# Kernel tuning notes

Measured on AMD Instinct MI355X. Metric: run time of the kernel, lower is better.

## Reference

```python
import jax, jax.numpy as jnp
import numpy as np

NUM_HEADS = 8
NUM_LEVEL = 4
KERNEL = 2
NUM_POINT = KERNEL * KERNEL
D_MODEL = 256
HEAD_DIM = D_MODEL // NUM_HEADS
REF_SIZE = 4
EPS = 1e-6


def _kernel_indices():
    # even kernel: linspace(-k/2+0.5, k/2-0.5, k) -> [-0.5, 0.5] for k=2
    ind = np.linspace(-KERNEL // 2 + 0.5, KERNEL // 2 - 0.5, KERNEL)
    i, j = np.meshgrid(ind, ind, indexing='ij')
    ki = np.stack([j, i], axis=-1).reshape(-1, 2) / KERNEL  # (P, 2), (x, y)
    return jnp.asarray(ki, dtype=jnp.float32)


def _ref_windows(shapes):
    # mask is None -> centers on a regular grid, size = ref_size / (H, W)
    refs = []
    for (H, W) in shapes:
        y = (jnp.arange(1, H + 1, dtype=jnp.float32) - 0.5) / (H + EPS)
        x = (jnp.arange(1, W + 1, dtype=jnp.float32) - 0.5) / (W + EPS)
        yy, xx = jnp.meshgrid(y, x, indexing='ij')           # (H, W)
        center = jnp.stack([xx, yy], axis=-1).reshape(-1, 2)  # (HW, 2)
        size = jnp.broadcast_to(
            jnp.array([REF_SIZE / W, REF_SIZE / H], dtype=jnp.float32), center.shape)
        refs.append(jnp.concatenate([center, size], axis=-1))
    return jnp.concatenate(refs, axis=0)  # (L, 4)


def _bilinear_sample(vflat, grid, H, W):
    """vflat: (B, H*W, M, D) one level; grid: (B, Lq, M, P, 2) normalized [0,1].
    Returns (B, Lq, M, P, D). Zero padding outside, align_corners=False."""
    B, _, M, D = vflat.shape
    x = grid[..., 0] * W - 0.5
    y = grid[..., 1] * H - 0.5
    x0 = jnp.floor(x); y0 = jnp.floor(y)
    lx = x - x0; ly = y - y0
    x0i = x0.astype(jnp.int32); y0i = y0.astype(jnp.int32)
    bidx = jnp.arange(B)[:, None, None, None]
    midx = jnp.arange(M)[None, None, :, None]

    def corner(xi, yi, w):
        valid = (xi >= 0) & (xi < W) & (yi >= 0) & (yi < H)
        idx = jnp.clip(yi, 0, H - 1) * W + jnp.clip(xi, 0, W - 1)
        g = vflat[bidx, idx, midx]  # (B, Lq, M, P, D)
        return g * (w * valid.astype(w.dtype))[..., None]

    out = corner(x0i, y0i, (1 - lx) * (1 - ly))
    out = out + corner(x0i + 1, y0i, lx * (1 - ly))
    out = out + corner(x0i, y0i + 1, (1 - lx) * ly)
    out = out + corner(x0i + 1, y0i + 1, lx * ly)
    return out


def setup_inputs() -> dict:
    key = jax.random.key(0)
    ks = jax.random.split(key, 20)
    spatial = [(100, 100), (50, 50), (25, 25), (13, 13)]
    B = 4
    inp = {}
    for i, (H, W) in enumerate(spatial):
        inp[f'value{i}'] = jax.random.normal(ks[i], (B, D_MODEL, H, W), dtype=jnp.float32)
        inp[f'pos{i}'] = jax.random.normal(ks[4 + i], (B, D_MODEL, H, W), dtype=jnp.float32)
    s = 0.05
    inp['Wv'] = jax.random.normal(ks[8], (D_MODEL, D_MODEL), dtype=jnp.float32) * s
    inp['bv'] = jnp.zeros((D_MODEL,), dtype=jnp.float32)
    inp['Wo'] = jax.random.normal(ks[9], (D_MODEL, D_MODEL), dtype=jnp.float32) * s
    inp['bo'] = jnp.zeros((D_MODEL,), dtype=jnp.float32)
    nb = NUM_LEVEL * NUM_HEADS * 4
    inp['Wbox'] = jax.random.normal(ks[10], (nb, D_MODEL), dtype=jnp.float32) * s
    inp['bbox'] = jax.random.uniform(ks[11], (nb,), dtype=jnp.float32)
    na = NUM_HEADS * NUM_LEVEL * NUM_POINT
    inp['Wattn'] = jax.random.normal(ks[12], (na, D_MODEL), dtype=jnp.float32) * s
    inp['battn'] = jax.random.normal(ks[13], (na,), dtype=jnp.float32) * s
    return inp


def reference(value0, value1, value2, value3, pos0, pos1, pos2, pos3,
              Wv, bv, Wo, bo, Wbox, bbox, Wattn, battn):
    levels = [value0, value1, value2, value3]
    poss = [pos0, pos1, pos2, pos3]
    shapes = [(v.shape[2], v.shape[3]) for v in levels]
    B = levels[0].shape[0]

    # flatten pyramid: (B, C, H, W) -> (B, HW, C)
    value = jnp.concatenate(
        [v.reshape(B, D_MODEL, -1).transpose(0, 2, 1) for v in levels], axis=1)
    pos = jnp.concatenate(
        [p.reshape(B, D_MODEL, -1).transpose(0, 2, 1) for p in poss], axis=1)
    L = value.shape[1]

    query = value + pos
    vp = (value @ Wv.T + bv).reshape(B, L, NUM_HEADS, HEAD_DIM)

    attn = jax.nn.softmax(
        (query @ Wattn.T + battn).reshape(B, L, NUM_HEADS, NUM_LEVEL * NUM_POINT),
        axis=-1).reshape(B, L, NUM_HEADS, NUM_LEVEL, NUM_POINT)

    offset = (query @ Wbox.T + bbox).reshape(B, L, NUM_HEADS, NUM_LEVEL, 4)
    ref = _ref_windows(shapes)[None, :, None, None, :]          # (1, L, 1, 1, 4)
    boxes = ref + offset / 8.0 * ref[..., jnp.array([2, 3, 2, 3])]
    center = boxes[..., None, :2]                               # (B, L, M, NL, 1, 2)
    size = boxes[..., None, 2:]
    ki = _kernel_indices()[None, None, None, None, :, :]        # (1,1,1,1,P,2)
    grid = center + ki * jax.nn.relu(size)                      # (B, L, M, NL, P, 2)

    out = jnp.zeros((B, L, NUM_HEADS, HEAD_DIM), dtype=vp.dtype)
    start = 0
    for l, (H, W) in enumerate(shapes):
        end = start + H * W
        vf = vp[:, start:end]                                   # (B, HW, M, D)
        sampled = _bilinear_sample(vf, grid[:, :, :, l], H, W)  # (B, L, M, P, D)
        out = out + jnp.einsum('blmp,blmpd->blmd', attn[:, :, :, l], sampled)
        start = end

    return out.reshape(B, L, D_MODEL) @ Wo.T + bo
```

## Files before the change

### kernel.cpp

```cpp
#include <hip/hip_runtime.h>
#include <cstdint>
#include <cmath>

#define D_MODEL 256
#define NH 8
#define NLVL 4
#define LTOT 13294
#define BATCH 4
#define BTOT (BATCH * LTOT)
#define RPAD 53248

typedef __attribute__((ext_vector_type(8))) short bf8;
typedef __attribute__((ext_vector_type(4))) float f4;
typedef __attribute__((ext_vector_type(2))) float f2;

__device__ __forceinline__ unsigned short f2bf(float x) {
    unsigned u = __float_as_uint(x);
    u += 0x7fffu + ((u >> 16) & 1u);
    return (unsigned short)(u >> 16);
}
__device__ __forceinline__ float bf2f(unsigned short h) {
    return __uint_as_float(((unsigned)h) << 16);
}
__device__ __forceinline__ f2 up2(unsigned u) {
    return (f2){__uint_as_float(u << 16), __uint_as_float(u & 0xffff0000u)};
}
__device__ __forceinline__ int swzf(int i, int s) { return s ^ ((i >> 1) & 3); }
__device__ __forceinline__ int xcd_swz(int hw, int nwg) {
    int xcd = hw & 7, k = hw >> 3;
    int q = nwg >> 3, r = nwg & 7;
    return (xcd < r ? xcd * (q + 1) : r * (q + 1) + (xcd - r) * q) + k;
}

__device__ __forceinline__ void level_of(int l, int& lv, int& hw, int& Wl, int& HWl, int& loff) {
    if (l < 10000)      { lv = 0; loff = 0;     Wl = 100; HWl = 10000; }
    else if (l < 12500) { lv = 1; loff = 10000; Wl = 50;  HWl = 2500;  }
    else if (l < 13125) { lv = 2; loff = 12500; Wl = 25;  HWl = 625;   }
    else                { lv = 3; loff = 13125; Wl = 13;  HWl = 169;   }
    hw = l - loff;
}

__global__ __launch_bounds__(256) void pack_weights(
    const float* __restrict__ Wv, const float* __restrict__ Wattn,
    const float* __restrict__ Wbox, const float* __restrict__ Wo,
    unsigned short* __restrict__ W1hi, unsigned short* __restrict__ W1lo,
    unsigned short* __restrict__ Wohi, unsigned short* __restrict__ Wolo) {
    int tid = blockIdx.x * 256 + threadIdx.x;
    const float* src;
    unsigned short *dh, *dl;
    int nb, kb, j, s;
    if (tid < 16384) {
        nb = tid >> 12; kb = (tid >> 9) & 7; j = (tid >> 2) & 127; s = tid & 3;
        int f = nb * 128 + j, c0 = kb * 32 + s * 8;
        if (f < 256)      src = Wv + (size_t)f * 256 + c0;
        else if (f < 384) src = Wattn + (size_t)(f - 256) * 256 + c0;
        else              src = Wbox + (size_t)(f - 384) * 256 + c0;
        dh = W1hi; dl = W1lo;
    } else if (tid < 24576) {
        int t2 = tid - 16384;
        nb = t2 >> 12; kb = (t2 >> 9) & 7; j = (t2 >> 2) & 127; s = t2 & 3;
        int f = nb * 128 + j, c0 = kb * 32 + s * 8;
        src = Wo + (size_t)f * 256 + c0;
        dh = Wohi; dl = Wolo;
    } else return;
    int base = (((nb * 8 + kb) * 128 + j) * 4 + swzf(j, s)) * 8;
    #pragma unroll
    for (int e = 0; e < 8; ++e) {
        float x = src[e];
        unsigned short h = f2bf(x);
        dh[base + e] = h;
        dl[base + e] = f2bf(x - bf2f(h));
    }
}

__global__ __launch_bounds__(256) void convert_A(
    const float* __restrict__ v0, const float* __restrict__ v1,
    const float* __restrict__ v2, const float* __restrict__ v3,
    const float* __restrict__ p0, const float* __restrict__ p1,
    const float* __restrict__ p2, const float* __restrict__ p3,
    unsigned short* __restrict__ Gv, unsigned short* __restrict__ Gq) {
    __shared__ unsigned short HV[64][130];
    __shared__ unsigned short HQ[64][130];
    int t = threadIdx.x;
    int w = t >> 6, lane = t & 63;
    int r0 = blockIdx.x * 64;

    int r = r0 + lane; if (r >= BTOT) r = BTOT - 1;
    int b = r / LTOT, l = r % LTOT;
    int lv, hw, Wl, HWl, loff;
    level_of(l, lv, hw, Wl, HWl, loff);
    const float *vb, *pb;
    switch (lv) { case 0: vb = v0; pb = p0; break; case 1: vb = v1; pb = p1; break;
                  case 2: vb = v2; pb = p2; break; default: vb = v3; pb = p3; break; }
    size_t base = (size_t)b * D_MODEL * (size_t)HWl + (size_t)hw;
    vb += base; pb += base;

    int kb2 = (lane >> 2) & 3, slot = lane & 3;
    for (int h = 0; h < 2; ++h) {
        #pragma unroll 4
        for (int i = 0; i < 32; ++i) {
            int cl = i * 4 + w;
            int c = h * 128 + cl;
            float av = vb[(size_t)c * HWl];
            float aq = av + pb[(size_t)c * HWl];
            HV[lane][cl] = f2bf(av);
            HQ[lane][cl] = f2bf(aq);
        }
        __syncthreads();
        #pragma unroll
        for (int j = 0; j < 8; ++j) {
            int plane = j >> 2;
            int rl = (j & 3) * 16 + w * 4 + (lane >> 4);
            int oct = slot ^ ((rl >> 1) & 3);
            const unsigned* s32 = (const unsigned*)(plane ? &HQ[rl][kb2 * 32 + oct * 8]
                                                          : &HV[rl][kb2 * 32 + oct * 8]);
            uint4 vst = make_uint4(s32[0], s32[1], s32[2], s32[3]);
            unsigned short* dst = (plane ? Gq : Gv)
                + (size_t)(r0 + rl) * 256 + (h * 4 + kb2) * 32 + slot * 8;
            *(uint4*)dst = vst;
        }
        __syncthreads();
    }
}

__global__ __launch_bounds__(512, 4) void gemm1_mfma(
    const unsigned short* __restrict__ Gv, const unsigned short* __restrict__ Gq,
    const unsigned short* __restrict__ W1hi, const unsigned short* __restrict__ W1lo,
    const float* __restrict__ bv, const float* __restrict__ battn, const float* __restrict__ bbox,
    unsigned short* __restrict__ VPb, float* __restrict__ LB) {
    __shared__ __align__(16) unsigned short Ah[2][8192], Bh[2][4096], Bl[2][4096];
    int t = threadIdx.x;
    int lid = xcd_swz(blockIdx.x, 4 * (RPAD / 256));
    int nb = lid & 3;
    int r0 = (lid >> 2) * 256;
    const unsigned short* Asrc = (nb < 2) ? Gv : Gq;
    int w = t >> 6, lane = t & 63;
    int wr = w >> 1, wc = w & 1;
    int row_l = lane & 15, oct = lane >> 4;

    const unsigned short* Bbh = W1hi + (size_t)nb * 32768;
    const unsigned short* Bbl = W1lo + (size_t)nb * 32768;

    f4 acc[4][4];
    #pragma unroll
    for (int i = 0; i < 4; ++i)
        #pragma unroll
        for (int j = 0; j < 4; ++j) acc[i][j] = (f4){0.f, 0.f, 0.f, 0.f};

    int c0 = t, c1 = t + 512;
    const unsigned short* a0b = Asrc + (size_t)(r0 + (c0 >> 2)) * 256 + (c0 & 3) * 8;
    const unsigned short* a1b = Asrc + (size_t)(r0 + (c1 >> 2)) * 256 + (c1 & 3) * 8;

#define G1_STAGE(bb, kb)                                                            \
    {                                                                               \
        __builtin_amdgcn_global_load_lds(a0b + (kb) * 32, &Ah[bb][w * 512], 16, 0, 0);        \
        __builtin_amdgcn_global_load_lds(a1b + (kb) * 32, &Ah[bb][4096 + w * 512], 16, 0, 0); \
        __builtin_amdgcn_global_load_lds(Bbh + (kb) * 4096 + c0 * 8, &Bh[bb][w * 512], 16, 0, 0); \
        __builtin_amdgcn_global_load_lds(Bbl + (kb) * 4096 + c0 * 8, &Bl[bb][w * 512], 16, 0, 0); \
    }

    G1_STAGE(0, 0);
    for (int kb = 0; kb < 8; ++kb) {
        __syncthreads();
        if (kb < 7) G1_STAGE((kb + 1) & 1, kb + 1);
        int bb = kb & 1;
        bf8 a[4], bh[4], bl[4];
        #pragma unroll
        for (int x = 0; x < 4; ++x) {
            int ri = wr * 64 + x * 16 + row_l;
            int ci = wc * 64 + x * 16 + row_l;
            a[x]  = *(const bf8*)(&Ah[bb][ri * 32 + swzf(ri, oct) * 8]);
            bh[x] = *(const bf8*)(&Bh[bb][ci * 32 + swzf(ci, oct) * 8]);
            bl[x] = *(const bf8*)(&Bl[bb][ci * 32 + swzf(ci, oct) * 8]);
        }
        #pragma unroll
        for (int mi = 0; mi < 4; ++mi)
            #pragma unroll
            for (int ni = 0; ni < 4; ++ni) {
                f4 c = acc[mi][ni];
                c = __builtin_amdgcn_mfma_f32_16x16x32_bf16(a[mi], bh[ni], c, 0, 0, 0);
                c = __builtin_amdgcn_mfma_f32_16x16x32_bf16(a[mi], bl[ni], c, 0, 0, 0);
                acc[mi][ni] = c;
            }
    }
    #pragma unroll
    for (int ni = 0; ni < 4; ++ni) {
        int col = wc * 64 + ni * 16 + row_l;
        float bias;
        if (nb == 0) bias = bv[col];
        else if (nb == 1) bias = bv[128 + col];
        else if (nb == 2) bias = battn[col];
        else bias = bbox[col];
        #pragma unroll
        for (int mi = 0; mi < 4; ++mi) {
            #pragma unroll
            for (int v = 0; v < 4; ++v) {
                int rr = r0 + wr * 64 + mi * 16 + oct * 4 + v;
                if (rr < BTOT) {
                    float val = acc[mi][ni][v] + bias;
                    if (nb < 2) VPb[(size_t)rr * 256 + nb * 128 + col] = f2bf(val);
                    else        LB[(size_t)rr * 256 + (nb - 2) * 128 + col] = val;
                }
            }
        }
    }
}

__global__ __launch_bounds__(256) void sampler_kernel(const unsigned short* __restrict__ VPb,
                                                      const float* __restrict__ LB,
                                                      unsigned short* __restrict__ att_hi,
                                                      unsigned short* __restrict__ att_lo) {
    __shared__ float sw[64][128];
    const int Ws2[4]   = {100, 50, 25, 13};
    const int offs2[4] = {0, 10000, 12500, 13125};
    int t = threadIdx.x;
    int blk = xcd_swz(blockIdx.x, (BTOT * NH) / 64);

    #pragma unroll
    for (int pass = 0; pass < 4; ++pass) {
        int g = (t >> 4) + pass * 16;
        int p = t & 15;
        int grp = blk * 64 + g;
        int m = grp & 7;
        int r = grp >> 3;
        int l = r % LTOT;
        int rb0 = r - l;

        int lv, hw, Wl, HWl, loff;
        level_of(l, lv, hw, Wl, HWl, loff);
        int x, y;
        switch (lv) {
            case 0:  y = hw / 100; x = hw - y * 100; break;
            case 1:  y = hw / 50;  x = hw - y * 50;  break;
            case 2:  y = hw / 25;  x = hw - y * 25;  break;
            default: y = hw / 13;  x = hw - y * 13;  break;
        }
        float denom = (float)((double)Wl + 1e-6);
        float cx = ((float)x + 0.5f) / denom;
        float cy = ((float)y + 0.5f) / denom;
        float rsw = 4.0f / (float)Wl;

        const float* Lrow = LB + (size_t)r * 256;
        float lg = Lrow[m * 16 + p];
        float mx = lg;
        #pragma unroll
        for (int off = 8; off >= 1; off >>= 1)
            mx = fmaxf(mx, __shfl_xor(mx, off, 16));
        float e = __expf(lg - mx);
        float ssum = e;
        #pragma unroll
        for (int off = 8; off >= 1; off >>= 1)
            ssum += __shfl_xor(ssum, off, 16);
        float aw = e / ssum;

        int lp = p >> 2, pp = p & 3;
        int W2 = Ws2[lp];
        float fW2 = (float)W2;
        float o0 = Lrow[128 + m * 16 + lp * 4 + 0];
        float o1 = Lrow[128 + m * 16 + lp * 4 + 1];
        float o2 = Lrow[128 + m * 16 + lp * 4 + 2];
        float o3 = Lrow[128 + m * 16 + lp * 4 + 3];
        float bcx = cx + o0 * 0.125f * rsw;
        float bcy = cy + o1 * 0.125f * rsw;
        float bsx = fmaxf(fmaf(o2 * 0.125f, rsw, rsw), 0.f);
        float bsy = fmaxf(fmaf(o3 * 0.125f, rsw, rsw), 0.f);
        float kx = (pp & 1)  ? 0.25f : -0.25f;
        float ky = (pp >> 1) ? 0.25f : -0.25f;
        float xs = fmaf(bcx + kx * bsx, fW2, -0.5f);
        float ys = fmaf(bcy + ky * bsy, fW2, -0.5f);
        float x0f = floorf(xs), y0f = floorf(ys);
        float lx = xs - x0f, ly = ys - y0f;
        int x0 = (int)x0f, y0 = (int)y0f;
        int x1 = x0 + 1, y1 = y0 + 1;
        bool vx0 = (x0 >= 0) & (x0 < W2), vx1 = (x1 >= 0) & (x1 < W2);
        bool vy0 = (y0 >= 0) & (y0 < W2), vy1 = (y1 >= 0) & (y1 < W2);
        int x0c = min(max(x0, 0), W2 - 1), x1c = min(max(x1, 0), W2 - 1);
        int y0c = min(max(y0, 0), W2 - 1), y1c = min(max(y1, 0), W2 - 1);
        float w00 = (vx0 & vy0) ? aw * (1.f - lx) * (1.f - ly) : 0.f;
        float w01 = (vx1 & vy0) ? aw * lx * (1.f - ly) : 0.f;
        float w10 = (vx0 & vy1) ? aw * (1.f - lx) * ly : 0.f;
        float w11 = (vx1 & vy1) ? aw * lx * ly : 0.f;
        int rowb = rb0 + offs2[lp];
        int col  = m * 32;
        int i00 = ((rowb + y0c * W2 + x0c) * 256 + col) * 2;
        int i01 = ((rowb + y0c * W2 + x1c) * 256 + col) * 2;
        int i10 = ((rowb + y1c * W2 + x0c) * 256 + col) * 2;
        int i11 = ((rowb + y1c * W2 + x1c) * 256 + col) * 2;
        float* dst = &sw[g][(p ^ (g & 3)) << 3];
        *(float4*)dst       = (float4){w00, w01, w10, w11};
        *(float4*)(dst + 4) = (float4){__int_as_float(i00), __int_as_float(i01),
                                       __int_as_float(i10), __int_as_float(i11)};
    }
    __syncthreads();

    int g = t >> 2, lane4 = t & 3;
    unsigned dby = (unsigned)lane4 * 16u;
    const char* Vb = (const char*)VPb;
    f2 a01 = {0.f, 0.f}, a23 = {0.f, 0.f}, a45 = {0.f, 0.f}, a67 = {0.f, 0.f};
    #pragma unroll
    for (int p = 0; p < 16; ++p) {
        const float* sp = &sw[g][(p ^ (g & 3)) << 3];
        float4 wv = *(const float4*)sp;
        float4 fi = *(const float4*)(sp + 4);
        uint4 u00 = *(const uint4*)(Vb + (size_t)(__float_as_uint(fi.x) + dby));
        uint4 u01 = *(const uint4*)(Vb + (size_t)(__float_as_uint(fi.y) + dby));
        uint4 u10 = *(const uint4*)(Vb + (size_t)(__float_as_uint(fi.z) + dby));
        uint4 u11 = *(const uint4*)(Vb + (size_t)(__float_as_uint(fi.w) + dby));
        f2 w0 = {wv.x, wv.x}, w1 = {wv.y, wv.y}, w2 = {wv.z, wv.z}, w3 = {wv.w, wv.w};
        a01 = __builtin_elementwise_fma(w0, up2(u00.x), a01);
        a23 = __builtin_elementwise_fma(w0, up2(u00.y), a23);
        a45 = __builtin_elementwise_fma(w0, up2(u00.z), a45);
        a67 = __builtin_elementwise_fma(w0, up2(u00.w), a67);
        a01 = __builtin_elementwise_fma(w1, up2(u01.x), a01);
        a23 = __builtin_elementwise_fma(w1, up2(u01.y), a23);
        a45 = __builtin_elementwise_fma(w1, up2(u01.z), a45);
        a67 = __builtin_elementwise_fma(w1, up2(u01.w), a67);
        a01 = __builtin_elementwise_fma(w2, up2(u10.x), a01);
        a23 = __builtin_elementwise_fma(w2, up2(u10.y), a23);
        a45 = __builtin_elementwise_fma(w2, up2(u10.z), a45);
        a67 = __builtin_elementwise_fma(w2, up2(u10.w), a67);
        a01 = __builtin_elementwise_fma(w3, up2(u11.x), a01);
        a23 = __builtin_elementwise_fma(w3, up2(u11.y), a23);
        a45 = __builtin_elementwise_fma(w3, up2(u11.z), a45);
        a67 = __builtin_elementwise_fma(w3, up2(u11.w), a67);
    }
    int grp = blk * 64 + g;
    int m2 = grp & 7, r2 = grp >> 3;
    int slot = lane4 ^ ((r2 >> 1) & 3);
    size_t base = (size_t)r2 * 256 + m2 * 32 + slot * 8;
    float av[8] = {a01.x, a01.y, a23.x, a23.y, a45.x, a45.y, a67.x, a67.y};
    unsigned hp[4], lp4[4];
    #pragma unroll
    for (int q = 0; q < 4; ++q) {
        unsigned short h0 = f2bf(av[q * 2]), h1 = f2bf(av[q * 2 + 1]);
        unsigned short l0 = f2bf(av[q * 2] - bf2f(h0)), l1 = f2bf(av[q * 2 + 1] - bf2f(h1));
        hp[q]  = ((unsigned)h1 << 16) | h0;
        lp4[q] = ((unsigned)l1 << 16) | l0;
    }
    *(uint4*)&att_hi[base] = make_uint4(hp[0], hp[1], hp[2], hp[3]);
    *(uint4*)&att_lo[base] = make_uint4(lp4[0], lp4[1], lp4[2], lp4[3]);
}

__global__ __launch_bounds__(256) void gemm2_mfma(
    const unsigned short* __restrict__ Ahi_g, const unsigned short* __restrict__ Alo_g,
    const unsigned short* __restrict__ Wohi, const unsigned short* __restrict__ Wolo,
    const float* __restrict__ bo, float* __restrict__ out) {
    __shared__ __align__(16) unsigned short Ah[2][4096], Al[2][4096], Bh[2][4096], Bl[2][4096];
    int t = threadIdx.x;
    int lid = xcd_swz(blockIdx.x, 2 * ((BTOT + 127) / 128));
    int nb = lid & 1;
    int r0 = (lid >> 1) * 128;
    int w = t >> 6, lane = t & 63;
    int wr = w >> 1, wc = w & 1;
    int row_l = lane & 15, oct = lane >> 4;

    const unsigned short* Bbh = Wohi + (size_t)nb * 32768;
    const unsigned short* Bbl = Wolo + (size_t)nb * 32768;

    f4 acc[4][4];
    #pragma unroll
    for (int i = 0; i < 4; ++i)
        #pragma unroll
        for (int j = 0; j < 4; ++j) acc[i][j] = (f4){0.f, 0.f, 0.f, 0.f};

    int c0 = w * 64 + lane, c1 = c0 + 256;
    int ra0 = r0 + (c0 >> 2); if (ra0 >= BTOT) ra0 = BTOT - 1;
    int ra1 = r0 + (c1 >> 2); if (ra1 >= BTOT) ra1 = BTOT - 1;
    const unsigned short* ah0 = Ahi_g + (size_t)ra0 * 256 + (c0 & 3) * 8;
    const unsigned short* ah1 = Ahi_g + (size_t)ra1 * 256 + (c1 & 3) * 8;
    const unsigned short* al0 = Alo_g + (size_t)ra0 * 256 + (c0 & 3) * 8;
    const unsigned short* al1 = Alo_g + (size_t)ra1 * 256 + (c1 & 3) * 8;

#define G2_STAGE(bb, kb)                                                            \
    {                                                                               \
        __builtin_amdgcn_global_load_lds(ah0 + (kb) * 32, &Ah[bb][w * 512], 16, 0, 0);        \
        __builtin_amdgcn_global_load_lds(ah1 + (kb) * 32, &Ah[bb][2048 + w * 512], 16, 0, 0); \
        __builtin_amdgcn_global_load_lds(al0 + (kb) * 32, &Al[bb][w * 512], 16, 0, 0);        \
        __builtin_amdgcn_global_load_lds(al1 + (kb) * 32, &Al[bb][2048 + w * 512], 16, 0, 0); \
        __builtin_amdgcn_global_load_lds(Bbh + (kb) * 4096 + c0 * 8, &Bh[bb][w * 512], 16, 0, 0);        \
        __builtin_amdgcn_global_load_lds(Bbh + (kb) * 4096 + c1 * 8, &Bh[bb][2048 + w * 512], 16, 0, 0); \
        __builtin_amdgcn_global_load_lds(Bbl + (kb) * 4096 + c0 * 8, &Bl[bb][w * 512], 16, 0, 0);        \
        __builtin_amdgcn_global_load_lds(Bbl + (kb) * 4096 + c1 * 8, &Bl[bb][2048 + w * 512], 16, 0, 0); \
    }

    G2_STAGE(0, 0);
    for (int kb = 0; kb < 8; ++kb) {
        __syncthreads();
        if (kb < 7) G2_STAGE((kb + 1) & 1, kb + 1);
        int bb = kb & 1;
        bf8 ah[4], al[4], bh[4], bl[4];
        #pragma unroll
        for (int x = 0; x < 4; ++x) {
            int ri = wr * 64 + x * 16 + row_l;
            int ci = wc * 64 + x * 16 + row_l;
            ah[x] = *(const bf8*)(&Ah[bb][ri * 32 + swzf(ri, oct) * 8]);
            al[x] = *(const bf8*)(&Al[bb][ri * 32 + swzf(ri, oct) * 8]);
            bh[x] = *(const bf8*)(&Bh[bb][ci * 32 + swzf(ci, oct) * 8]);
            bl[x] = *(const bf8*)(&Bl[bb][ci * 32 + swzf(ci, oct) * 8]);
        }
        #pragma unroll
        for (int mi = 0; mi < 4; ++mi)
            #pragma unroll
            for (int ni = 0; ni < 4; ++ni) {
                f4 c = acc[mi][ni];
                c = __builtin_amdgcn_mfma_f32_16x16x32_bf16(ah[mi], bh[ni], c, 0, 0, 0);
                c = __builtin_amdgcn_mfma_f32_16x16x32_bf16(ah[mi], bl[ni], c, 0, 0, 0);
                c = __builtin_amdgcn_mfma_f32_16x16x32_bf16(al[mi], bh[ni], c, 0, 0, 0);
                acc[mi][ni] = c;
            }
    }
    #pragma unroll
    for (int ni = 0; ni < 4; ++ni) {
        int col = wc * 64 + ni * 16 + row_l;
        float bias = bo[nb * 128 + col];
        #pragma unroll
        for (int mi = 0; mi < 4; ++mi) {
            #pragma unroll
            for (int v = 0; v < 4; ++v) {
                int rr = r0 + wr * 64 + mi * 16 + oct * 4 + v;
                if (rr < BTOT)
                    out[(size_t)rr * 256 + nb * 128 + col] = acc[mi][ni][v] + bias;
            }
        }
    }
}

extern "C" void kernel_launch(void* const* d_in, const int* in_sizes, int n_in,
                              void* d_out, int out_size, void* d_ws, size_t ws_size,
                              hipStream_t stream) {
    const float* v0 = (const float*)d_in[0];
    const float* p0 = (const float*)d_in[1];
    const float* v1 = (const float*)d_in[2];
    const float* p1 = (const float*)d_in[3];
    const float* v2 = (const float*)d_in[4];
    const float* p2 = (const float*)d_in[5];
    const float* v3 = (const float*)d_in[6];
    const float* p3 = (const float*)d_in[7];
    const float* Wv    = (const float*)d_in[8];
    const float* bv    = (const float*)d_in[9];
    const float* Wo    = (const float*)d_in[10];
    const float* bo    = (const float*)d_in[11];
    const float* Wbox  = (const float*)d_in[12];
    const float* bbox  = (const float*)d_in[13];
    const float* Wattn = (const float*)d_in[14];
    const float* battn = (const float*)d_in[15];
    float* out = (float*)d_out;

    char* ws = (char*)d_ws;
    unsigned short* W1hi = (unsigned short*)(ws);
    unsigned short* W1lo = (unsigned short*)(ws + 262144);
    unsigned short* Wohi = (unsigned short*)(ws + 524288);
    unsigned short* Wolo = (unsigned short*)(ws + 655360);
    unsigned short* Gv   = (unsigned short*)(ws + 1048576);
    unsigned short* Gq   = (unsigned short*)(ws + 1048576 + 27262976);
    unsigned short* atth = Gv;
    unsigned short* attl = Gq;
    unsigned short* VPb  = (unsigned short*)(ws + 1048576 + 2 * 27262976);
    float*          LB   = (float*)(ws + 1048576 + 2 * 27262976 + 27226112);

    convert_A<<<dim3(RPAD / 64), dim3(256), 0, stream>>>(v0, v1, v2, v3,
                                                         p0, p1, p2, p3, Gv, Gq);
    pack_weights<<<dim3(96), dim3(256), 0, stream>>>(Wv, Wattn, Wbox, Wo,
                                                     W1hi, W1lo, Wohi, Wolo);

    gemm1_mfma<<<dim3(4 * (RPAD / 256)), dim3(512), 0, stream>>>(
        Gv, Gq, W1hi, W1lo, bv, battn, bbox, VPb, LB);

    sampler_kernel<<<dim3((BTOT * NH) / 64), dim3(256), 0, stream>>>(VPb, LB, atth, attl);

    gemm2_mfma<<<dim3(2 * ((BTOT + 127) / 128)), dim3(256), 0, stream>>>(
        atth, attl, Wohi, Wolo, bo, out);
}
```

Baseline: 217.2 us.

## Merge weight packing into conversion kernel and enlarge gemm2 tile to 256 rows

Weight packing now runs as extra blocks of the activation conversion kernel, which removes one kernel launch. The output GEMM moves from 128-row tiles with 256 threads to 256-row tiles with 512 threads. The B (weight) tile is now loaded once per 256 rows instead of once per 128, which halves weight traffic per output row, and the grid becomes smaller. The larger tile also doubles the A shared-memory buffers, which could reduce occupancy. The hidden epilogue and MFMA loop must map the 8 waves correctly for this to stay correct.

```diff
diff --git a/kernel.cpp b/kernel.cpp
--- a/kernel.cpp
+++ b/kernel.cpp
@@ -40,48 +40,50 @@
     hw = l - loff;
 }
 
-__global__ __launch_bounds__(256) void pack_weights(
-    const float* __restrict__ Wv, const float* __restrict__ Wattn,
-    const float* __restrict__ Wbox, const float* __restrict__ Wo,
-    unsigned short* __restrict__ W1hi, unsigned short* __restrict__ W1lo,
-    unsigned short* __restrict__ Wohi, unsigned short* __restrict__ Wolo) {
-    int tid = blockIdx.x * 256 + threadIdx.x;
-    const float* src;
-    unsigned short *dh, *dl;
-    int nb, kb, j, s;
-    if (tid < 16384) {
-        nb = tid >> 12; kb = (tid >> 9) & 7; j = (tid >> 2) & 127; s = tid & 3;
-        int f = nb * 128 + j, c0 = kb * 32 + s * 8;
-        if (f < 256)      src = Wv + (size_t)f * 256 + c0;
-        else if (f < 384) src = Wattn + (size_t)(f - 256) * 256 + c0;
-        else              src = Wbox + (size_t)(f - 384) * 256 + c0;
-        dh = W1hi; dl = W1lo;
-    } else if (tid < 24576) {
-        int t2 = tid - 16384;
-        nb = t2 >> 12; kb = (t2 >> 9) & 7; j = (t2 >> 2) & 127; s = t2 & 3;
-        int f = nb * 128 + j, c0 = kb * 32 + s * 8;
-        src = Wo + (size_t)f * 256 + c0;
-        dh = Wohi; dl = Wolo;
-    } else return;
-    int base = (((nb * 8 + kb) * 128 + j) * 4 + swzf(j, s)) * 8;
-    #pragma unroll
-    for (int e = 0; e < 8; ++e) {
-        float x = src[e];
-        unsigned short h = f2bf(x);
-        dh[base + e] = h;
-        dl[base + e] = f2bf(x - bf2f(h));
-    }
-}
-
-__global__ __launch_bounds__(256) void convert_A(
+__global__ __launch_bounds__(256) void convert_pack(
     const float* __restrict__ v0, const float* __restrict__ v1,
     const float* __restrict__ v2, const float* __restrict__ v3,
     const float* __restrict__ p0, const float* __restrict__ p1,
     const float* __restrict__ p2, const float* __restrict__ p3,
-    unsigned short* __restrict__ Gv, unsigned short* __restrict__ Gq) {
+    const float* __restrict__ Wv, const float* __restrict__ Wattn,
+    const float* __restrict__ Wbox, const float* __restrict__ Wo,
+    unsigned short* __restrict__ Gv, unsigned short* __restrict__ Gq,
+    unsigned short* __restrict__ W1hi, unsigned short* __restrict__ W1lo,
+    unsigned short* __restrict__ Wohi, unsigned short* __restrict__ Wolo) {
     __shared__ unsigned short HV[64][130];
     __shared__ unsigned short HQ[64][130];
     int t = threadIdx.x;
+
+    if (blockIdx.x >= RPAD / 64) {
+        int tid = (blockIdx.x - RPAD / 64) * 256 + t;
+        const float* src;
+        unsigned short *dh, *dl;
+        int nb, kb, j, s;
+        if (tid < 16384) {
+            nb = tid >> 12; kb = (tid >> 9) & 7; j = (tid >> 2) & 127; s = tid & 3;
+            int f = nb * 128 + j, c0 = kb * 32 + s * 8;
+            if (f < 256)      src = Wv + (size_t)f * 256 + c0;
+            else if (f < 384) src = Wattn + (size_t)(f - 256) * 256 + c0;
+            else              src = Wbox + (size_t)(f - 384) * 256 + c0;
+            dh = W1hi; dl = W1lo;
+        } else {
+            int t2 = tid - 16384;
+            nb = t2 >> 12; kb = (t2 >> 9) & 7; j = (t2 >> 2) & 127; s = t2 & 3;
+            int f = nb * 128 + j, c0 = kb * 32 + s * 8;
+            src = Wo + (size_t)f * 256 + c0;
+            dh = Wohi; dl = Wolo;
+        }
+        int base = (((nb * 8 + kb) * 128 + j) * 4 + swzf(j, s)) * 8;
+        #pragma unroll
+        for (int e = 0; e < 8; ++e) {
+            float x = src[e];
+            unsigned short h = f2bf(x);
+            dh[base + e] = h;
+            dl[base + e] = f2bf(x - bf2f(h));
+        }
+        return;
+    }
+
     int w = t >> 6, lane = t & 63;
     int r0 = blockIdx.x * 64;
 
@@ -341,15 +343,15 @@
     *(uint4*)&att_lo[base] = make_uint4(lp4[0], lp4[1], lp4[2], lp4[3]);
 }
 
-__global__ __launch_bounds__(256) void gemm2_mfma(
+__global__ __launch_bounds__(512, 2) void gemm2_mfma(
     const unsigned short* __restrict__ Ahi_g, const unsigned short* __restrict__ Alo_g,
     const unsigned short* __restrict__ Wohi, const unsigned short* __restrict__ Wolo,
     const float* __restrict__ bo, float* __restrict__ out) {
-    __shared__ __align__(16) unsigned short Ah[2][4096], Al[2][4096], Bh[2][4096], Bl[2][4096];
+    __shared__ __align__(16) unsigned short Ah[2][8192], Al[2][8192], Bh[2][4096], Bl[2][4096];
     int t = threadIdx.x;
-    int lid = xcd_swz(blockIdx.x, 2 * ((BTOT + 127) / 128));
+    int lid = xcd_swz(blockIdx.x, 2 * (RPAD / 256));
     int nb = lid & 1;
-    int r0 = (lid >> 1) * 128;
+    int r0 = (lid >> 1) * 256;
     int w = t >> 6, lane = t & 63;
     int wr = w >> 1, wc = w & 1;
     int row_l = lane & 15, oct = lane >> 4;
@@ -363,7 +365,7 @@
         #pragma unroll
         for (int j = 0; j < 4; ++j) acc[i][j] = (f4){0.f, 0.f, 0.f, 0.f};
 
-    int c0 = w * 64 + lane, c1 = c0 + 256;
+    int c0 = t, c1 = t + 512;
     int ra0 = r0 + (c0 >> 2); if (ra0 >= BTOT) ra0 = BTOT - 1;
     int ra1 = r0 + (c1 >> 2); if (ra1 >= BTOT) ra1 = BTOT - 1;
     const unsigned short* ah0 = Ahi_g + (size_t)ra0 * 256 + (c0 & 3) * 8;
@@ -374,13 +376,11 @@
 #define G2_STAGE(bb, kb)                                                            \
     {                                                                               \
         __builtin_amdgcn_global_load_lds(ah0 + (kb) * 32, &Ah[bb][w * 512], 16, 0, 0);        \
-        __builtin_amdgcn_global_load_lds(ah1 + (kb) * 32, &Ah[bb][2048 + w * 512], 16, 0, 0); \
+        __builtin_amdgcn_global_load_lds(ah1 + (kb) * 32, &Ah[bb][4096 + w * 512], 16, 0, 0); \
         __builtin_amdgcn_global_load_lds(al0 + (kb) * 32, &Al[bb][w * 512], 16, 0, 0);        \
-        __builtin_amdgcn_global_load_lds(al1 + (kb) * 32, &Al[bb][2048 + w * 512], 16, 0, 0); \
-        __builtin_amdgcn_global_load_lds(Bbh + (kb) * 4096 + c0 * 8, &Bh[bb][w * 512], 16, 0, 0);        \
-        __builtin_amdgcn_global_load_lds(Bbh + (kb) * 4096 + c1 * 8, &Bh[bb][2048 + w * 512], 16, 0, 0); \
-        __builtin_amdgcn_global_load_lds(Bbl + (kb) * 4096 + c0 * 8, &Bl[bb][w * 512], 16, 0, 0);        \
-        __builtin_amdgcn_global_load_lds(Bbl + (kb) * 4096 + c1 * 8, &Bl[bb][2048 + w * 512], 16, 0, 0); \
+        __builtin_amdgcn_global_load_lds(al1 + (kb) * 32, &Al[bb][4096 + w * 512], 16, 0, 0); \
+        __builtin_amdgcn_global_load_lds(Bbh + (kb) * 4096 + c0 * 8, &Bh[bb][w * 512], 16, 0, 0); \
+        __builtin_amdgcn_global_load_lds(Bbl + (kb) * 4096 + c0 * 8, &Bl[bb][w * 512], 16, 0, 0); \
     }
 
     G2_STAGE(0, 0);
@@ -458,16 +458,15 @@
     unsigned short* VPb  = (unsigned short*)(ws + 1048576 + 2 * 27262976);
     float*          LB   = (float*)(ws + 1048576 + 2 * 27262976 + 27226112);
 
-    convert_A<<<dim3(RPAD / 64), dim3(256), 0, stream>>>(v0, v1, v2, v3,
-                                                         p0, p1, p2, p3, Gv, Gq);
-    pack_weights<<<dim3(96), dim3(256), 0, stream>>>(Wv, Wattn, Wbox, Wo,
-                                                     W1hi, W1lo, Wohi, Wolo);
+    convert_pack<<<dim3(RPAD / 64 + 96), dim3(256), 0, stream>>>(
+        v0, v1, v2, v3, p0, p1, p2, p3, Wv, Wattn, Wbox, Wo,
+        Gv, Gq, W1hi, W1lo, Wohi, Wolo);
 
     gemm1_mfma<<<dim3(4 * (RPAD / 256)), dim3(512), 0, stream>>>(
         Gv, Gq, W1hi, W1lo, bv, battn, bbox, VPb, LB);
 
     sampler_kernel<<<dim3((BTOT * NH) / 64), dim3(256), 0, stream>>>(VPb, LB, atth, attl);
 
-    gemm2_mfma<<<dim3(2 * ((BTOT + 127) / 128)), dim3(256), 0, stream>>>(
+    gemm2_mfma<<<dim3(2 * (RPAD / 256)), dim3(512), 0, stream>>>(
         atth, attl, Wohi, Wolo, bo, out);
 }
```

Result: no change. 216.5 us (-0.3%).
